# Performance work log

Hardware: AMD Instinct MI355X
Metric: run time of the kernel (lower is better)

The kernel has to match this reference:

```python
import jax, jax.numpy as jnp
import numpy as np

B, L, DIM, H, D, WS = 2, 2048, 1024, 16, 64, 256
SCALE = D ** -0.5


def _rope_tables(seq_len, dim, dtype):
    inv_freq = 1.0 / (10000.0 ** (jnp.arange(0, dim, 2, dtype=jnp.float32) / dim))
    t = jnp.arange(seq_len, dtype=jnp.float32)
    freqs = jnp.einsum('i,j->ij', t, inv_freq)          # [L, D/2]
    emb = jnp.concatenate([freqs, freqs], axis=-1)       # [L, D]
    return jnp.cos(emb).astype(dtype), jnp.sin(emb).astype(dtype)


def _rotate_half(x):
    x1, x2 = x[..., : x.shape[-1] // 2], x[..., x.shape[-1] // 2:]
    return jnp.concatenate([-x2, x1], axis=-1)


def _apply_rope(t, cos, sin):
    # t: [B, L, H, D]; cos/sin: [L, D] broadcast over batch and heads
    return t * cos[None, :, None, :] + _rotate_half(t) * sin[None, :, None, :]


def setup_inputs() -> dict:
    key = jax.random.key(0)
    k0, k1, k2 = jax.random.split(key, 3)
    x = jax.random.normal(k0, (B, L, DIM), dtype=jnp.float32)
    Wqkv = jax.random.normal(k1, (3 * H * D, DIM), dtype=jnp.float32) * 0.02
    bqkv = jnp.zeros((3 * H * D,), dtype=jnp.float32)
    Wproj = jax.random.normal(k2, (DIM, H * D), dtype=jnp.float32) * 0.02
    bproj = jnp.zeros((DIM,), dtype=jnp.float32)
    return {"x": x, "Wqkv": Wqkv, "bqkv": bqkv, "Wproj": Wproj, "bproj": bproj, "is_global": 1}


def _attention(x, Wqkv, bqkv, Wproj, bproj, is_global):
    b, l, _ = x.shape
    qkv = x @ Wqkv.T + bqkv                              # [B, L, 3*H*D]
    q, k, v = jnp.split(qkv, 3, axis=-1)
    q, k, v = (t.reshape(b, l, H, D) for t in (q, k, v))
    cos, sin = _rope_tables(l, D, x.dtype)
    q = _apply_rope(q, cos, sin)
    k = _apply_rope(k, cos, sin)
    if is_global:
        attn = jnp.einsum('bshd,bthd->bhst', q, k) * SCALE
        attn = jax.nn.softmax(attn, axis=-1)
        out = jnp.einsum('bhst,bthd->bshd', attn, v)     # [B, L, H, D]
    else:
        pad = (WS - l % WS) % WS
        if pad > 0:
            q, k, v = (jnp.pad(t, ((0, 0), (0, pad), (0, 0), (0, 0))) for t in (q, k, v))
        w = (l + pad) // WS
        q = q.reshape(b, w, WS, H, D)
        k = k.reshape(b, w, WS, H, D)
        v = v.reshape(b, w, WS, H, D)
        attn = jnp.einsum('bwshd,bwthd->bwhst', q, k) * SCALE
        attn = jax.nn.softmax(attn, axis=-1)
        out = jnp.einsum('bwhst,bwthd->bwshd', attn, v).reshape(b, w * WS, H, D)
        out = out[:, :l]
    return out.reshape(b, l, H * D) @ Wproj.T + bproj


def reference(x, Wqkv, bqkv, Wproj, bproj, is_global):
    return _attention(x, Wqkv, bqkv, Wproj, bproj, is_global)
```

## Files before the change

kernel.cpp:

```cpp
#include <hip/hip_runtime.h>
#include <math.h>

#define NB 2
#define NL 2048
#define NDIM 1024
#define NH 16
#define ND 64
#define NWS 256
#define NM (NB*NL)
#define QSCALE 0.18033688011112042f

typedef __attribute__((ext_vector_type(8))) short short8;
typedef __attribute__((ext_vector_type(4))) float f32x4;
typedef unsigned short ushort_t;
typedef unsigned int uint_t;

#define MFMA16(a,b,acc) __builtin_amdgcn_mfma_f32_16x16x32_bf16((a),(b),(acc),0,0,0)

static __device__ __forceinline__ ushort_t f2bf(float x){
    uint_t u = __float_as_uint(x);
    uint_t r = (u + 0x7fff + ((u >> 16) & 1)) >> 16;
    return (ushort_t)r;
}
static __device__ __forceinline__ float bf2f(ushort_t u){
    return __uint_as_float(((uint_t)u) << 16);
}
static __device__ __forceinline__ float fast_exp2(float x){
#if __has_builtin(__builtin_amdgcn_exp2f)
    return __builtin_amdgcn_exp2f(x);
#else
    return exp2f(x);
#endif
}

static __device__ __forceinline__ void async_load16(const void* g, void* l){
    __builtin_amdgcn_global_load_lds(
        (const __attribute__((address_space(1))) unsigned int*)g,
        (__attribute__((address_space(3))) unsigned int*)l, 16, 0, 0);
}

__launch_bounds__(256)
__global__ void split_hl(const float* __restrict__ in, ushort_t* __restrict__ oh,
                         ushort_t* __restrict__ ol)
{
    const int i = (blockIdx.x*256 + threadIdx.x)*4;
    const float4 v = *(const float4*)(in + i);
    ushort_t h0=f2bf(v.x), h1=f2bf(v.y), h2=f2bf(v.z), h3=f2bf(v.w);
    ushort4 h4; h4.x=h0; h4.y=h1; h4.z=h2; h4.w=h3;
    ushort4 l4;
    l4.x=f2bf(v.x - bf2f(h0)); l4.y=f2bf(v.y - bf2f(h1));
    l4.z=f2bf(v.z - bf2f(h2)); l4.w=f2bf(v.w - bf2f(h3));
    *(ushort4*)(oh + i) = h4;
    *(ushort4*)(ol + i) = l4;
}

__launch_bounds__(256)
__global__ void rope_tab(float* __restrict__ tc, float* __restrict__ ts)
{
    const int idx = blockIdx.x*256 + threadIdx.x;
    const int j = idx >> 11, l = idx & (NL-1);
    const float invf = 1.0f / powf(10000.0f, (float)j * (1.0f/32.0f));
    float s, c;
    sincosf((float)l * invf, &s, &c);
    tc[idx] = c; ts[idx] = s;
}

template<int MODE>
__launch_bounds__(256, (MODE==0) ? 3 : 4)
__global__ void gemm_hl(const ushort_t* __restrict__ Ah, const ushort_t* __restrict__ Al,
                        const ushort_t* __restrict__ Bh, const ushort_t* __restrict__ Bl,
                        const float* __restrict__ bias,
                        float* __restrict__ Cout,
                        ushort_t* __restrict__ oQh, ushort_t* __restrict__ oKh,
                        ushort_t* __restrict__ oVth,
                        const float* __restrict__ tcos, const float* __restrict__ tsin)
{
    __shared__ __align__(16) char smem[(MODE==0) ? 50176 : 32768];
    ushort_t* sA_h = (ushort_t*)smem;
    ushort_t* sA_l = (ushort_t*)(smem + 8192);
    ushort_t* sB_h = (ushort_t*)(smem + 16384);
    ushort_t* sB_l = (MODE==1) ? (ushort_t*)(smem + 24576) : sB_h;
    ushort_t* sBounce = (ushort_t*)smem;
    const int ebuf = 12288;
    const int bbuf = 24576;

    const int tid  = threadIdx.x;
    const int wv   = tid >> 6, lane = tid & 63;
    const int quad = lane >> 4, l16 = lane & 15;
    const int m0 = blockIdx.y << 7, n0 = blockIdx.x << 7;
    const int wr = wv >> 1, wc = wv & 1;

    const ushort_t* gsrc;
    ushort_t* lds_base;
    int rowb, npass;
    if (MODE == 1) {
        gsrc = (wv==0)?Ah:(wv==1)?Al:(wv==2)?Bh:Bl;
        lds_base = (wv==0)?sA_h:(wv==1)?sA_l:(wv==2)?sB_h:sB_l;
        rowb = (wv < 2) ? m0 : n0;
        npass = 8;
    } else {
        if (wv == 0)      { gsrc = Ah; lds_base = sA_h; rowb = m0; npass = 8; }
        else if (wv == 1) { gsrc = Al; lds_base = sA_l; rowb = m0; npass = 8; }
        else { gsrc = Bh; lds_base = sB_h + (wv-2)*64*32; rowb = n0 + (wv-2)*64; npass = 4; }
    }
    const int rl = lane >> 2;
    const int cp = lane & 3;
    const int cg = cp ^ ((rl >> 1) & 3);
    const ushort_t* gptr = gsrc + (size_t)(rowb + rl)*NDIM + cg*8;

    f32x4 acc[4][4];
    #pragma unroll
    for (int i=0;i<4;++i)
        #pragma unroll
        for (int j=0;j<4;++j) acc[i][j] = (f32x4){0.f,0.f,0.f,0.f};

    const int swz = (l16 >> 1) & 3;
    const int ac_off = (wr*64 + l16)*32 + ((quad ^ swz) << 3);
    const int bc_off = (wc*64 + l16)*32 + ((quad ^ swz) << 3);

#define GSTAGE(BUF, KOFF) do { \
        const ushort_t* gp_ = gptr + (KOFF); \
        for (int p=0; p<npass; ++p) \
            async_load16(gp_ + (size_t)p*16*NDIM, (char*)lds_base + (BUF)*bbuf + p*1024); \
    } while(0)

#define GCOMP(BUF) do { \
        const int eo_ = (BUF)*ebuf; \
        short8 ah[4], al[4], bh[4], bl[4]; \
        _Pragma("unroll") \
        for (int t=0;t<4;++t){ \
            ah[t] = *(const short8*)&sA_h[eo_ + t*512 + ac_off]; \
            al[t] = *(const short8*)&sA_l[eo_ + t*512 + ac_off]; \
            bh[t] = *(const short8*)&sB_h[eo_ + t*512 + bc_off]; \
            if (MODE == 1) bl[t] = *(const short8*)&sB_l[eo_ + t*512 + bc_off]; \
        } \
        _Pragma("unroll") \
        for (int mt=0;mt<4;++mt) \
            _Pragma("unroll") \
            for (int nt=0;nt<4;++nt){ \
                f32x4 a_ = acc[mt][nt]; \
                a_ = MFMA16(ah[mt], bh[nt], a_); \
                a_ = MFMA16(al[mt], bh[nt], a_); \
                if (MODE == 1) a_ = MFMA16(ah[mt], bl[nt], a_); \
                acc[mt][nt] = a_; \
            } \
    } while(0)

    if (MODE == 0) {
        GSTAGE(0, 0);
        for (int k0 = 0; k0 < NDIM; k0 += 64) {
            __syncthreads();
            GSTAGE(1, k0 + 32);
            GCOMP(0);
            __syncthreads();
            if (k0 + 64 < NDIM) GSTAGE(0, k0 + 64);
            GCOMP(1);
        }
    } else {
        for (int k0 = 0; k0 < NDIM; k0 += 32) {
            __syncthreads();
            GSTAGE(0, k0);
            __syncthreads();
            GCOMP(0);
        }
    }
#undef GSTAGE
#undef GCOMP

    if (MODE == 1) {
        const int colb = n0 + wc*64;
        float bq[4];
        #pragma unroll
        for (int nt=0;nt<4;++nt) bq[nt] = bias[colb + nt*16 + l16];
        #pragma unroll
        for (int mt=0;mt<4;++mt)
            #pragma unroll
            for (int r=0;r<4;++r){
                const int m = m0 + wr*64 + mt*16 + quad*4 + r;
                float* orow = Cout + (size_t)m*NDIM + colb;
                #pragma unroll
                for (int nt=0;nt<4;++nt)
                    orow[nt*16 + l16] = acc[mt][nt][r] + bq[nt];
            }
    } else {
        const int colb = n0 + wc*64;
        const int sel  = colb >> 10;
        const int head = (colb & 1023) >> 6;
        float bq[4];
        #pragma unroll
        for (int nt=0;nt<4;++nt) bq[nt] = bias[colb + nt*16 + l16];

        if (sel == 2) {
            __syncthreads();
            const int bb = m0 >> 11;
            const int Lb = (m0 & (NL-1)) + wr*64;
            ushort_t* sT = sBounce + wv*(64*72);
            const size_t gb = ((size_t)(bb*NH + head)*ND)*NL + Lb;
            const int drow = lane >> 3, dcol = lane & 7;
            #pragma unroll
            for (int mt=0;mt<4;++mt)
                #pragma unroll
                for (int nt=0;nt<4;++nt)
                    #pragma unroll
                    for (int r=0;r<4;++r)
                        sT[(nt*16+l16)*72 + mt*16 + quad*4 + r] = f2bf(acc[mt][nt][r] + bq[nt]);
            #pragma unroll
            for (int dd=0; dd<8; ++dd){
                const int d = dd*8 + drow;
                const uint4 v = *(const uint4*)&sT[d*72 + dcol*8];
                *(uint4*)(oVth + gb + (size_t)d*NL + dcol*8) = v;
            }
        } else {
            ushort_t* dh = sel ? oKh : oQh;
            const float qs = sel ? 1.0f : QSCALE;
            #pragma unroll
            for (int mt=0;mt<4;++mt)
                #pragma unroll
                for (int r=0;r<4;++r){
                    const int m = m0 + wr*64 + mt*16 + quad*4 + r;
                    const int bb = m >> 11, l = m & (NL-1);
                    const size_t ro = ((size_t)((bb*NH + head)*NL + l)) << 6;
                    #pragma unroll
                    for (int ntp=0;ntp<2;++ntp){
                        const int j = ntp*16 + l16;
                        const float c = tcos[j*NL + l];
                        const float s = tsin[j*NL + l];
                        const float x1 = acc[mt][ntp  ][r] + bq[ntp];
                        const float x2 = acc[mt][ntp+2][r] + bq[ntp+2];
                        const int d1 = ntp*16 + l16;
                        dh[ro + d1]      = f2bf((x1*c - x2*s) * qs);
                        dh[ro + d1 + 32] = f2bf((x2*c + x1*s) * qs);
                    }
                }
        }
    }
}

__launch_bounds__(256, 4)
__global__ void attn_mfma(const ushort_t* __restrict__ Qh,
                          const ushort_t* __restrict__ Kh,
                          const ushort_t* __restrict__ Vth,
                          ushort_t* __restrict__ AOh, ushort_t* __restrict__ AOl,
                          const int* __restrict__ isg)
{
    __shared__ __align__(16) char smem[40960];

    const int tid  = threadIdx.x;
    const int wv   = tid >> 6, lane = tid & 63;
    const int quad = lane >> 4, l16 = lane & 15;
    const int bh = blockIdx.x & 31, qt = blockIdx.x >> 5;
    const int q0w = qt*64 + wv*16;

    short8 bq0, bq1;
    {
        const size_t rb = (((size_t)bh*NL + q0w) << 6) + (size_t)(l16 << 6) + quad*8;
        bq0 = *(const short8*)(Qh + rb);
        bq1 = *(const short8*)(Qh + rb + 32);
    }
    short8 ones;
    #pragma unroll
    for (int j=0;j<8;++j) ones[j] = (short)0x3F80;

    f32x4 o[4];
    #pragma unroll
    for (int dnt=0; dnt<4; ++dnt) o[dnt] = (f32x4){0.f,0.f,0.f,0.f};
    f32x4 lsacc = (f32x4){0.f,0.f,0.f,0.f};

    const int gflag = isg[0];
    int klo, khi;
    if (gflag) { klo = 0; khi = NL; }
    else       { klo = (qt >> 2)*NWS; khi = klo + NWS; }

    const int swz4 = (l16 & 7) << 4;
    const int KC0 = l16*128 + (( quad*16      ) ^ swz4);
    const int KC1 = l16*128 + (( quad*16 + 64 ) ^ swz4);
    const int sPb = 32768 + wv*2048;
    int PW[4];
    #pragma unroll
    for (int knt=0; knt<4; ++knt)
        PW[knt] = sPb + l16*128 + ((knt*32 + quad*8) ^ swz4);
    const int PR0 = sPb + KC0;
    const int PR1 = sPb + KC1;

    const int r8  = lane >> 3;
    const int c8s = (lane & 7) ^ r8;
    const ushort_t* Kp = Kh + (((size_t)bh*NL) << 6)
                       + (size_t)(klo + wv*16 + r8)*64 + c8s*8;
    const ushort_t* Vp = Vth + (size_t)bh*ND*NL
                       + (size_t)(wv*16 + r8)*NL + klo + c8s*8;
    const int kdst = wv*2048;
    const int vdst = 16384 + wv*2048;

#define STAGE(BUF) do { \
        async_load16(Kp,          smem + (BUF)*8192 + kdst); \
        async_load16(Kp + 512,    smem + (BUF)*8192 + kdst + 1024); \
        async_load16(Vp,          smem + (BUF)*8192 + vdst); \
        async_load16(Vp + 8*NL,   smem + (BUF)*8192 + vdst + 1024); \
        Kp += 64*64; Vp += 64; } while (0)

#define TILE(BUF) do { \
        const char* kb_ = smem + (BUF)*8192; \
        const char* vb_ = smem + 16384 + (BUF)*8192; \
        f32x4 s_[4]; \
        _Pragma("unroll") \
        for (int knt=0; knt<4; ++knt) { \
            const short8 a0 = *(const short8*)(kb_ + knt*2048 + KC0); \
            const short8 a1 = *(const short8*)(kb_ + knt*2048 + KC1); \
            f32x4 t = (f32x4){0.f,0.f,0.f,0.f}; \
            t = MFMA16(a0, bq0, t); \
            t = MFMA16(a1, bq1, t); \
            s_[knt] = t; \
        } \
        _Pragma("unroll") \
        for (int knt=0; knt<4; ++knt) { \
            const uint_t u0 = __float_as_uint(fast_exp2(s_[knt][0])); \
            const uint_t u1 = __float_as_uint(fast_exp2(s_[knt][1])); \
            const uint_t u2 = __float_as_uint(fast_exp2(s_[knt][2])); \
            const uint_t u3 = __float_as_uint(fast_exp2(s_[knt][3])); \
            uint2 pk_; \
            pk_.x = __builtin_amdgcn_perm(u1, u0, 0x07060302u); \
            pk_.y = __builtin_amdgcn_perm(u3, u2, 0x07060302u); \
            *(uint2*)(smem + PW[knt]) = pk_; \
        } \
        const short8 fp0 = *(const short8*)(smem + PR0); \
        const short8 fp1 = *(const short8*)(smem + PR1); \
        lsacc = MFMA16(fp0, ones, lsacc); \
        lsacc = MFMA16(fp1, ones, lsacc); \
        _Pragma("unroll") \
        for (int dnt=0; dnt<4; ++dnt) { \
            const short8 v0 = *(const short8*)(vb_ + dnt*2048 + KC0); \
            const short8 v1 = *(const short8*)(vb_ + dnt*2048 + KC1); \
            f32x4 t = o[dnt]; \
            t = MFMA16(fp0, v0, t); \
            t = MFMA16(fp1, v1, t); \
            o[dnt] = t; \
        } } while (0)

    STAGE(0);
    for (int kt = klo; kt < khi; kt += 128) {
        __syncthreads();
        if (kt + 64 < khi) STAGE(1);
        TILE(0);
        __syncthreads();
        if (kt + 128 < khi) STAGE(0);
        TILE(1);
    }
#undef STAGE
#undef TILE

    const int bb = bh >> 4, hh = bh & 15;
    #pragma unroll
    for (int r=0; r<4; ++r) {
        const float inv = 1.0f / lsacc[r];
        const int row = q0w + quad*4 + r;
        const size_t ob = (((size_t)(bb*NL + row)) << 10) + (hh << 6);
        #pragma unroll
        for (int dnt=0; dnt<4; ++dnt) {
            const float val = o[dnt][r] * inv;
            const ushort_t h = f2bf(val);
            AOh[ob + dnt*16 + l16] = h;
            AOl[ob + dnt*16 + l16] = f2bf(val - bf2f(h));
        }
    }
}

extern "C" void kernel_launch(void* const* d_in, const int* in_sizes, int n_in,
                              void* d_out, int out_size, void* d_ws, size_t ws_size,
                              hipStream_t stream)
{
    const float* x     = (const float*)d_in[0];
    const float* Wqkv  = (const float*)d_in[1];
    const float* bqkv  = (const float*)d_in[2];
    const float* Wproj = (const float*)d_in[3];
    const float* bproj = (const float*)d_in[4];
    const int*   isg   = (const int*)d_in[5];
    float* out = (float*)d_out;
    char* base = (char*)d_ws;

    const size_t MB = 1024*1024;
    ushort_t* Qh  = (ushort_t*)(base);
    ushort_t* Kh  = (ushort_t*)(base + 16*MB);
    ushort_t* Vth = (ushort_t*)(base + 32*MB);
    ushort_t* xh  = (ushort_t*)(base + 48*MB);
    ushort_t* xl  = (ushort_t*)(base + 56*MB);
    ushort_t* AOh = xh;
    ushort_t* AOl = xl;
    ushort_t* Wqh = (ushort_t*)(base + 64*MB);
    ushort_t* Wql = (ushort_t*)(base + 64*MB + 6291456);
    ushort_t* Wph = (ushort_t*)(base + 76*MB);
    ushort_t* Wpl = (ushort_t*)(base + 76*MB + 2097152);
    float*    tcs = (float*)(base + 80*MB);
    float*    tsn = (float*)(base + 80*MB + 262144);

    split_hl<<<4096, 256, 0, stream>>>(x, xh, xl);
    split_hl<<<3072, 256, 0, stream>>>(Wqkv, Wqh, Wql);
    split_hl<<<1024, 256, 0, stream>>>(Wproj, Wph, Wpl);
    rope_tab<<<256, 256, 0, stream>>>(tcs, tsn);

    gemm_hl<0><<<dim3(3*NDIM/128, NM/128), 256, 0, stream>>>(
        xh, xl, Wqh, Wql, bqkv, nullptr,
        Qh, Kh, Vth, tcs, tsn);

    attn_mfma<<<NB*NH*(NL/64), 256, 0, stream>>>(
        Qh, Kh, Vth, AOh, AOl, isg);

    gemm_hl<1><<<dim3(NDIM/128, NM/128), 256, 0, stream>>>(
        AOh, AOl, Wph, Wpl, bproj, out,
        nullptr, nullptr, nullptr, nullptr, nullptr);
}
```

Baseline: 232.6 us.

## Merge split kernels and retile output projection GEMM with double buffering

```diff
diff --git a/kernel.cpp b/kernel.cpp
--- a/kernel.cpp
+++ b/kernel.cpp
@@ -40,18 +40,24 @@
 }
 
 __launch_bounds__(256)
-__global__ void split_hl(const float* __restrict__ in, ushort_t* __restrict__ oh,
-                         ushort_t* __restrict__ ol)
+__global__ void split_all(const float* __restrict__ x,  ushort_t* __restrict__ xh,  ushort_t* __restrict__ xl,
+                          const float* __restrict__ wq, ushort_t* __restrict__ wqh, ushort_t* __restrict__ wql,
+                          const float* __restrict__ wp, ushort_t* __restrict__ wph, ushort_t* __restrict__ wpl)
 {
-    const int i = (blockIdx.x*256 + threadIdx.x)*4;
-    const float4 v = *(const float4*)(in + i);
+    int i = blockIdx.x*256 + threadIdx.x;
+    const float* in; ushort_t *oh, *ol;
+    if (i < 1048576)      { in = x;  oh = xh;  ol = xl;  }
+    else if (i < 1835008) { in = wq; oh = wqh; ol = wql; i -= 1048576; }
+    else                  { in = wp; oh = wph; ol = wpl; i -= 1835008; }
+    const int e = i*4;
+    const float4 v = *(const float4*)(in + e);
     ushort_t h0=f2bf(v.x), h1=f2bf(v.y), h2=f2bf(v.z), h3=f2bf(v.w);
     ushort4 h4; h4.x=h0; h4.y=h1; h4.z=h2; h4.w=h3;
     ushort4 l4;
     l4.x=f2bf(v.x - bf2f(h0)); l4.y=f2bf(v.y - bf2f(h1));
     l4.z=f2bf(v.z - bf2f(h2)); l4.w=f2bf(v.w - bf2f(h3));
-    *(ushort4*)(oh + i) = h4;
-    *(ushort4*)(ol + i) = l4;
+    *(ushort4*)(oh + e) = h4;
+    *(ushort4*)(ol + e) = l4;
 }
 
 __launch_bounds__(256)
@@ -66,7 +72,7 @@
 }
 
 template<int MODE>
-__launch_bounds__(256, (MODE==0) ? 3 : 4)
+__launch_bounds__(256, 3)
 __global__ void gemm_hl(const ushort_t* __restrict__ Ah, const ushort_t* __restrict__ Al,
                         const ushort_t* __restrict__ Bh, const ushort_t* __restrict__ Bl,
                         const float* __restrict__ bias,
@@ -75,19 +81,22 @@
                         ushort_t* __restrict__ oVth,
                         const float* __restrict__ tcos, const float* __restrict__ tsin)
 {
-    __shared__ __align__(16) char smem[(MODE==0) ? 50176 : 32768];
+    __shared__ __align__(16) char smem[50176];
     ushort_t* sA_h = (ushort_t*)smem;
     ushort_t* sA_l = (ushort_t*)(smem + 8192);
     ushort_t* sB_h = (ushort_t*)(smem + 16384);
-    ushort_t* sB_l = (MODE==1) ? (ushort_t*)(smem + 24576) : sB_h;
+    ushort_t* sB_l = (ushort_t*)(smem + 20480);
     ushort_t* sBounce = (ushort_t*)smem;
     const int ebuf = 12288;
     const int bbuf = 24576;
+    const int NTILE = (MODE==0) ? 128 : 64;
+    const int WN    = (MODE==0) ? 64  : 32;
+    const int NTT   = (MODE==0) ? 4   : 2;
 
     const int tid  = threadIdx.x;
     const int wv   = tid >> 6, lane = tid & 63;
     const int quad = lane >> 4, l16 = lane & 15;
-    const int m0 = blockIdx.y << 7, n0 = blockIdx.x << 7;
+    const int m0 = blockIdx.y << 7, n0 = blockIdx.x * NTILE;
     const int wr = wv >> 1, wc = wv & 1;
 
     const ushort_t* gsrc;
@@ -97,7 +106,7 @@
         gsrc = (wv==0)?Ah:(wv==1)?Al:(wv==2)?Bh:Bl;
         lds_base = (wv==0)?sA_h:(wv==1)?sA_l:(wv==2)?sB_h:sB_l;
         rowb = (wv < 2) ? m0 : n0;
-        npass = 8;
+        npass = (wv < 2) ? 8 : 4;
     } else {
         if (wv == 0)      { gsrc = Ah; lds_base = sA_h; rowb = m0; npass = 8; }
         else if (wv == 1) { gsrc = Al; lds_base = sA_l; rowb = m0; npass = 8; }
@@ -108,15 +117,15 @@
     const int cg = cp ^ ((rl >> 1) & 3);
     const ushort_t* gptr = gsrc + (size_t)(rowb + rl)*NDIM + cg*8;
 
-    f32x4 acc[4][4];
+    f32x4 acc[4][NTT];
     #pragma unroll
     for (int i=0;i<4;++i)
         #pragma unroll
-        for (int j=0;j<4;++j) acc[i][j] = (f32x4){0.f,0.f,0.f,0.f};
+        for (int j=0;j<NTT;++j) acc[i][j] = (f32x4){0.f,0.f,0.f,0.f};
 
     const int swz = (l16 >> 1) & 3;
     const int ac_off = (wr*64 + l16)*32 + ((quad ^ swz) << 3);
-    const int bc_off = (wc*64 + l16)*32 + ((quad ^ swz) << 3);
+    const int bc_off = (wc*WN + l16)*32 + ((quad ^ swz) << 3);
 
 #define GSTAGE(BUF, KOFF) do { \
         const ushort_t* gp_ = gptr + (KOFF); \
@@ -126,18 +135,21 @@
 
 #define GCOMP(BUF) do { \
         const int eo_ = (BUF)*ebuf; \
-        short8 ah[4], al[4], bh[4], bl[4]; \
+        short8 ah[4], al[4], bh[NTT], bl[NTT]; \
         _Pragma("unroll") \
         for (int t=0;t<4;++t){ \
             ah[t] = *(const short8*)&sA_h[eo_ + t*512 + ac_off]; \
             al[t] = *(const short8*)&sA_l[eo_ + t*512 + ac_off]; \
+        } \
+        _Pragma("unroll") \
+        for (int t=0;t<NTT;++t){ \
             bh[t] = *(const short8*)&sB_h[eo_ + t*512 + bc_off]; \
             if (MODE == 1) bl[t] = *(const short8*)&sB_l[eo_ + t*512 + bc_off]; \
         } \
         _Pragma("unroll") \
         for (int mt=0;mt<4;++mt) \
             _Pragma("unroll") \
-            for (int nt=0;nt<4;++nt){ \
+            for (int nt=0;nt<NTT;++nt){ \
                 f32x4 a_ = acc[mt][nt]; \
                 a_ = MFMA16(ah[mt], bh[nt], a_); \
                 a_ = MFMA16(al[mt], bh[nt], a_); \
@@ -146,32 +158,23 @@
             } \
     } while(0)
 
-    if (MODE == 0) {
-        GSTAGE(0, 0);
-        for (int k0 = 0; k0 < NDIM; k0 += 64) {
-            __syncthreads();
-            GSTAGE(1, k0 + 32);
-            GCOMP(0);
-            __syncthreads();
-            if (k0 + 64 < NDIM) GSTAGE(0, k0 + 64);
-            GCOMP(1);
-        }
-    } else {
-        for (int k0 = 0; k0 < NDIM; k0 += 32) {
-            __syncthreads();
-            GSTAGE(0, k0);
-            __syncthreads();
-            GCOMP(0);
-        }
+    GSTAGE(0, 0);
+    for (int k0 = 0; k0 < NDIM; k0 += 64) {
+        __syncthreads();
+        GSTAGE(1, k0 + 32);
+        GCOMP(0);
+        __syncthreads();
+        if (k0 + 64 < NDIM) GSTAGE(0, k0 + 64);
+        GCOMP(1);
     }
 #undef GSTAGE
 #undef GCOMP
 
     if (MODE == 1) {
-        const int colb = n0 + wc*64;
-        float bq[4];
+        const int colb = n0 + wc*32;
+        float bq[2];
         #pragma unroll
-        for (int nt=0;nt<4;++nt) bq[nt] = bias[colb + nt*16 + l16];
+        for (int nt=0;nt<2;++nt) bq[nt] = bias[colb + nt*16 + l16];
         #pragma unroll
         for (int mt=0;mt<4;++mt)
             #pragma unroll
@@ -179,7 +182,7 @@
                 const int m = m0 + wr*64 + mt*16 + quad*4 + r;
                 float* orow = Cout + (size_t)m*NDIM + colb;
                 #pragma unroll
-                for (int nt=0;nt<4;++nt)
+                for (int nt=0;nt<2;++nt)
                     orow[nt*16 + l16] = acc[mt][nt][r] + bq[nt];
             }
     } else {
@@ -392,9 +395,7 @@
     float*    tcs = (float*)(base + 80*MB);
     float*    tsn = (float*)(base + 80*MB + 262144);
 
-    split_hl<<<4096, 256, 0, stream>>>(x, xh, xl);
-    split_hl<<<3072, 256, 0, stream>>>(Wqkv, Wqh, Wql);
-    split_hl<<<1024, 256, 0, stream>>>(Wproj, Wph, Wpl);
+    split_all<<<8192, 256, 0, stream>>>(x, xh, xl, Wqkv, Wqh, Wql, Wproj, Wph, Wpl);
     rope_tab<<<256, 256, 0, stream>>>(tcs, tsn);
 
     gemm_hl<0><<<dim3(3*NDIM/128, NM/128), 256, 0, stream>>>(
@@ -404,7 +405,7 @@
     attn_mfma<<<NB*NH*(NL/64), 256, 0, stream>>>(
         Qh, Kh, Vth, AOh, AOl, isg);
 
-    gemm_hl<1><<<dim3(NDIM/128, NM/128), 256, 0, stream>>>(
+    gemm_hl<1><<<dim3(NDIM/64, NM/128), 256, 0, stream>>>(
         AOh, AOl, Wph, Wpl, bproj, out,
         nullptr, nullptr, nullptr, nullptr, nullptr);
 }
```

After: 231.0 us. Within noise of the previous version (-0.7%).
